# Optimization experiments

Measured on AMD Instinct MI355X. Metric: run time of the kernel, lower is better.

Reference implementation:

```python
import jax, jax.numpy as jnp
import numpy as np

# 4D convolution via lax.conv_general_dilated with 4 spatial dims.
# Layout: input (N, C, D, H, W, T), kernel (O, I, d, h, w, t).
DN = ('NCDHWT', 'OIDHWT', 'NCDHWT')


def conv4d(x, w, b, pad):
    # torch Conv2d/Conv4d is cross-correlation, matching lax.conv_general_dilated
    y = jax.lax.conv_general_dilated(
        x, w, window_strides=(1, 1, 1, 1),
        padding=[(pad, pad)] * 4, dimension_numbers=DN)
    return y + b.reshape(1, -1, 1, 1, 1, 1)


def _kaiming(key, shape):
    fan_out = shape[0] * int(np.prod(shape[2:]))
    std = np.sqrt(2.0 / fan_out)
    return (jax.random.normal(key, shape, dtype=jnp.float32) * std).astype(jnp.float32)


def setup_inputs() -> dict:
    key = jax.random.key(0)
    ks = jax.random.split(key, 11)
    B, W, H = 256, 16, 16
    corr = jax.random.normal(ks[0], (B, W * H, W, H), dtype=jnp.float32)
    w1 = _kaiming(ks[1], (1, 1, 17, 17, 9, 9))
    w2 = _kaiming(ks[2], (1, 1, 7, 7, 7, 7))
    w3 = _kaiming(ks[3], (1, 1, 5, 5, 5, 5))
    w4 = _kaiming(ks[4], (1, 1, 3, 3, 3, 3))
    w5 = _kaiming(ks[5], (1, 1, 8, 8, 1, 1))
    b1 = jax.random.normal(ks[6], (1,), dtype=jnp.float32) * 0.01
    b2 = jax.random.normal(ks[7], (1,), dtype=jnp.float32) * 0.01
    b3 = jax.random.normal(ks[8], (1,), dtype=jnp.float32) * 0.01
    b4 = jax.random.normal(ks[9], (1,), dtype=jnp.float32) * 0.01
    b5 = jax.random.normal(ks[10], (1,), dtype=jnp.float32) * 0.01
    return {"corr": corr, "w1": w1, "b1": b1, "w2": w2, "b2": b2,
            "w3": w3, "b3": b3, "w4": w4, "b4": b4, "w5": w5, "b5": b5}


def reference(corr, w1, b1, w2, b2, w3, b3, w4, b4, w5, b5):
    B, HW, W, H = corr.shape
    x = corr.reshape(B, 1, W, H, W, H)          # (B,1,16,16,16,16)
    x = jax.nn.relu(conv4d(x, w1, b1, 4))       # (B,1, 8, 8,16,16)
    x = jax.nn.relu(conv4d(x, w2, b2, 3))
    x = jax.nn.relu(conv4d(x, w3, b3, 2))
    x = jax.nn.relu(conv4d(x, w4, b4, 1))
    out = jax.nn.sigmoid(conv4d(x, w5, b5, 0))  # (B,1, 1, 1,16,16)
    return out.reshape(B, 1, W, H)
```

## Files before the change

### kernel.cpp

```cpp
#include <hip/hip_runtime.h>
#include <math.h>


typedef short bf16x8 __attribute__((ext_vector_type(8)));
typedef float f32x4 __attribute__((ext_vector_type(4)));
typedef unsigned int u32x4 __attribute__((ext_vector_type(4)));

#define XTS 64
#define NROWS 396
#define ZROW 384
#define TTS 72

__device__ __forceinline__ int xts(int row, int col) {
  return row * XTS + (col ^ ((row & 7) << 3));
}

__device__ __forceinline__ unsigned short f2bf(float f) {
  unsigned int u = __float_as_uint(f);
  u += 0x7fffu + ((u >> 16) & 1u);
  return (unsigned short)(u >> 16);
}

template <int KSZ, int PAD>
__device__ __forceinline__ void build_mid(const float* __restrict__ w,
                                          unsigned short* __restrict__ Bg, int gid) {
  const int lane = gid & 63;
  const int n_tile = (gid >> 6) & 3;
  const int chunk = (gid >> 8) & 1;
  const int tap = gid >> 9;
  const int kw = tap / KSZ, kt = tap - kw * KSZ;
  const int dh_o = n_tile * 16 + (lane & 15);
  const int d_o = dh_o >> 3, h_o = dh_o & 7;
  const int kbase = chunk * 32 + (lane >> 4) * 8;
  unsigned int pk[4];
#pragma unroll
  for (int p = 0; p < 4; ++p) {
    unsigned short half[2];
#pragma unroll
    for (int s = 0; s < 2; ++s) {
      const int k = kbase + p * 2 + s;
      const int d_i = k >> 3, h_i = k & 7;
      const int kd = d_i - d_o + PAD, kh = h_i - h_o + PAD;
      float v = 0.f;
      if (kd >= 0 && kd < KSZ && kh >= 0 && kh < KSZ)
        v = w[((kd * KSZ + kh) * KSZ + kw) * KSZ + kt];
      half[s] = f2bf(v);
    }
    pk[p] = (unsigned int)half[0] | ((unsigned int)half[1] << 16);
  }
  *(int4*)(Bg + (size_t)gid * 8) = make_int4(pk[0], pk[1], pk[2], pk[3]);
}

__global__ __launch_bounds__(256) void build_all(const float* __restrict__ w1,
                                                 const float* __restrict__ w2,
                                                 const float* __restrict__ w3,
                                                 const float* __restrict__ w4,
                                                 unsigned short* __restrict__ Bg1,
                                                 unsigned short* __restrict__ Bg2,
                                                 unsigned short* __restrict__ Bg3,
                                                 unsigned short* __restrict__ Bg4) {
  const int bid = blockIdx.x, tid = threadIdx.x;
  if (bid < 648) {
    const int gid = bid * 256 + tid;
    const int lane = gid & 63;
    const int n_tile = (gid >> 6) & 3;
    const int chunk = (gid >> 8) & 7;
    const int kwkt = gid >> 11;
    const int kw = kwkt / 9, kt = kwkt - kw * 9;
    const int dh_o = n_tile * 16 + (lane & 15);
    const int d_o = dh_o >> 3, h_o = dh_o & 7;
    const int kbase = chunk * 32 + (lane >> 4) * 8;
    unsigned int pk[4];
#pragma unroll
    for (int p = 0; p < 4; ++p) {
      unsigned short half[2];
#pragma unroll
      for (int s = 0; s < 2; ++s) {
        const int k = kbase + p * 2 + s;
        const int d_i = k >> 4, h_i = k & 15;
        const int kd = d_i - d_o + 4, kh = h_i - h_o + 4;
        float v = 0.f;
        if (kd >= 0 && kd < 17 && kh >= 0 && kh < 17)
          v = w1[((kd * 17 + kh) * 9 + kw) * 9 + kt];
        half[s] = f2bf(v);
      }
      pk[p] = (unsigned int)half[0] | ((unsigned int)half[1] << 16);
    }
    *(int4*)(Bg1 + (size_t)gid * 8) = make_int4(pk[0], pk[1], pk[2], pk[3]);
  } else if (bid < 746) {
    build_mid<7, 3>(w2, Bg2, (bid - 648) * 256 + tid);
  } else if (bid < 796) {
    build_mid<5, 2>(w3, Bg3, (bid - 746) * 256 + tid);
  } else {
    build_mid<3, 1>(w4, Bg4, (bid - 796) * 256 + tid);
  }
}

__device__ __forceinline__ void l1_load(const unsigned short* XT,
                                        const unsigned short* __restrict__ Bt,
                                        const int (&arb)[4], int kt,
                                        const int (&c0t)[8], const int (&c1t)[8],
                                        bf16x8 (&A)[8], bf16x8 (&B)[8]) {
#pragma unroll
  for (int m = 0; m < 4; ++m) {
    A[m] = *(const bf16x8*)&XT[arb[m] + kt * XTS + c0t[kt & 7]];
    A[4 + m] = *(const bf16x8*)&XT[arb[m] + kt * XTS + c1t[kt & 7]];
  }
#pragma unroll
  for (int c = 0; c < 2; ++c)
#pragma unroll
    for (int n = 0; n < 4; ++n)
      B[c * 4 + n] = *(const bf16x8*)(Bt + (size_t)kt * 16384 + c * 2048 + n * 512);
}

__device__ __forceinline__ void mfma16(const bf16x8 (&A)[8], const bf16x8 (&B)[8],
                                       f32x4 (&acc)[4][4]) {
  __builtin_amdgcn_s_setprio(1);
#pragma unroll
  for (int c = 0; c < 2; ++c)
#pragma unroll
    for (int m = 0; m < 4; ++m)
#pragma unroll
      for (int n = 0; n < 4; ++n)
        acc[m][n] = __builtin_amdgcn_mfma_f32_16x16x32_bf16(A[c * 4 + m], B[c * 4 + n],
                                                            acc[m][n], 0, 0, 0);
  __builtin_amdgcn_s_setprio(0);
}

__global__ __launch_bounds__(256) void conv_l1_mfma(const float* __restrict__ x,
                                                    const unsigned short* __restrict__ Bg,
                                                    float* __restrict__ P) {
  __shared__ __align__(16) unsigned short XT[NROWS * XTS];
  const int bx = blockIdx.x;
  const int b = bx >> 2, q = bx & 3;
  const int tid = threadIdx.x;
  const int lane = tid & 63, wave = tid >> 6;
  const int quad = lane >> 4, tl = lane & 15;
  const float* xb = x + (size_t)b * 65536;
  f32x4 acc[4][4] = {};

  int c0t[8], c1t[8];
#pragma unroll
  for (int j = 0; j < 8; ++j) {
    const int sw = ((tl + j) & 7) << 3;
    c0t[j] = (quad * 8) ^ sw;
    c1t[j] = (quad * 8 + 32) ^ sw;
  }

  for (int j = tid; j < (NROWS * XTS) / 8; j += 256)
    *(int4*)&XT[j * 8] = make_int4(0, 0, 0, 0);
  __syncthreads();

#pragma unroll
  for (int it = 0; it < 8; ++it) {
    const int i = tid + it * 256;
    const int dhp = i >> 6, wtq = i & 63;
    const int r0 = (wtq >> 2) * 24 + (wtq & 3) * 4 + 4;
    const float4 ra = *(const float4*)(xb + (size_t)(q * 64 + 2 * dhp) * 256 + wtq * 4);
    const float4 rb = *(const float4*)(xb + (size_t)(q * 64 + 2 * dhp + 1) * 256 + wtq * 4);
    const float a0[4] = {ra.x, ra.y, ra.z, ra.w};
    const float a1[4] = {rb.x, rb.y, rb.z, rb.w};
#pragma unroll
    for (int j = 0; j < 4; ++j) {
      const unsigned int p = (unsigned int)f2bf(a0[j]) | ((unsigned int)f2bf(a1[j]) << 16);
      *(unsigned int*)&XT[xts(r0 + j, dhp * 2)] = p;
    }
  }
  __syncthreads();

  const int chbase = q * 2;
  const unsigned short* Bt = Bg + (size_t)chbase * 2048 + lane * 8;
  for (int kw = 0; kw < 9; ++kw) {
    int arb[4];
#pragma unroll
    for (int m = 0; m < 4; ++m) {
      const int w_i = wave * 4 + m + kw - 4;
      arb[m] = (((unsigned)w_i < 16u) ? (w_i * 24 + tl) : ZROW) * XTS;
    }
    bf16x8 A0[8], B0[8], A1[8], B1[8];
    l1_load(XT, Bt, arb, 0, c0t, c1t, A0, B0);
#pragma unroll
    for (int kt = 0; kt < 9; ++kt) {
      if ((kt & 1) == 0) {
        if (kt < 8) l1_load(XT, Bt, arb, kt + 1, c0t, c1t, A1, B1);
        mfma16(A0, B0, acc);
      } else {
        if (kt < 8) l1_load(XT, Bt, arb, kt + 1, c0t, c1t, A0, B0);
        mfma16(A1, B1, acc);
      }
    }
    Bt += 9 * 16384;
  }

  float* Pb = P + (size_t)(q * 256 + b) * 16384;
#pragma unroll
  for (int m = 0; m < 4; ++m)
#pragma unroll
    for (int n = 0; n < 4; ++n) {
      const int dh_o = n * 16 + tl;
      const int wt0 = wave * 64 + m * 16 + quad * 4;
      *(float4*)&Pb[(size_t)dh_o * 256 + wt0] = *(const float4*)&acc[m][n];
    }
}

template <int KSZ, int PAD>
__device__ __forceinline__ void tail_load_tap(const unsigned short* XT,
                                              const unsigned short* __restrict__ Bg, int kwkt,
                                              int mw, int nh, int lane, int quad, int tl,
                                              bf16x8 (&A)[8], bf16x8 (&B)[4]) {
  const int kw = kwkt / KSZ, kt = kwkt - kw * KSZ;
  const int t_i = tl + kt - PAD;
  const bool tv = (unsigned)t_i < 16u;
  int ro[4];
#pragma unroll
  for (int m = 0; m < 4; ++m) {
    const int w_i = mw * 4 + m + kw - PAD;
    const bool v = tv && ((unsigned)w_i < 16u);
    const int row = v ? (w_i * 16 + t_i) : 256;
    ro[m] = row * TTS + quad * 8;
  }
#pragma unroll
  for (int c = 0; c < 2; ++c)
#pragma unroll
    for (int m = 0; m < 4; ++m)
      A[c * 4 + m] = *(const bf16x8*)&XT[ro[m] + c * 32];
#pragma unroll
  for (int c = 0; c < 2; ++c)
#pragma unroll
    for (int n = 0; n < 2; ++n)
      B[c * 2 + n] =
          *(const bf16x8*)(Bg + (((size_t)(kwkt * 2 + c) * 4 + (nh * 2 + n)) << 9) + lane * 8);
}

__device__ __forceinline__ void mfma8(const bf16x8 (&A)[8], const bf16x8 (&B)[4],
                                      f32x4 (&acc)[4][2]) {
  __builtin_amdgcn_s_setprio(1);
#pragma unroll
  for (int c = 0; c < 2; ++c)
#pragma unroll
    for (int m = 0; m < 4; ++m)
#pragma unroll
      for (int n = 0; n < 2; ++n)
        acc[m][n] = __builtin_amdgcn_mfma_f32_16x16x32_bf16(A[c * 4 + m], B[c * 2 + n],
                                                            acc[m][n], 0, 0, 0);
  __builtin_amdgcn_s_setprio(0);
}

template <int KSZ, int PAD, int NT>
__device__ __forceinline__ void run_layer(unsigned short* XT,
                                          const unsigned short* __restrict__ Bg,
                                          const float bias, int mw, int nh, int lane,
                                          int quad, int tl) {
  f32x4 acc[4][2] = {};
  {
    bf16x8 A0[8], B0[4], A1[8], B1[4];
    tail_load_tap<KSZ, PAD>(XT, Bg, 0, mw, nh, lane, quad, tl, A0, B0);
    int k = 0;
    while (true) {
      if (k + 1 < NT) tail_load_tap<KSZ, PAD>(XT, Bg, k + 1, mw, nh, lane, quad, tl, A1, B1);
      mfma8(A0, B0, acc);
      if (++k >= NT) break;
      if (k + 1 < NT) tail_load_tap<KSZ, PAD>(XT, Bg, k + 1, mw, nh, lane, quad, tl, A0, B0);
      mfma8(A1, B1, acc);
      if (++k >= NT) break;
    }
  }
  __syncthreads();
#pragma unroll
  for (int m = 0; m < 4; ++m)
#pragma unroll
    for (int n = 0; n < 2; ++n) {
      const int col = (nh * 2 + n) * 16 + tl;
      const int wt0 = mw * 64 + m * 16 + quad * 4;
#pragma unroll
      for (int j = 0; j < 4; ++j)
        XT[(wt0 + j) * TTS + col] = f2bf(fmaxf(acc[m][n][j] + bias, 0.f));
    }
  __syncthreads();
}

__global__ __launch_bounds__(512) void tail_fused(const float* __restrict__ P,
                                                  const unsigned short* __restrict__ Bg2,
                                                  const unsigned short* __restrict__ Bg3,
                                                  const unsigned short* __restrict__ Bg4,
                                                  const float* __restrict__ b1,
                                                  const float* __restrict__ b2,
                                                  const float* __restrict__ b3,
                                                  const float* __restrict__ b4,
                                                  const float* __restrict__ w5,
                                                  const float* __restrict__ b5,
                                                  float* __restrict__ out) {
  __shared__ __align__(16) unsigned short XT[257 * TTS];
  const int b = blockIdx.x;
  const int tid = threadIdx.x;
  const int lane = tid & 63, wave = tid >> 6;
  const int quad = lane >> 4, tl = lane & 15;
  const int mw = wave >> 1, nh = wave & 1;
  const float* p0 = P + (size_t)b * 16384;
  const float* p1 = p0 + (size_t)256 * 16384;
  const float* p2 = p0 + (size_t)512 * 16384;
  const float* p3 = p0 + (size_t)768 * 16384;
  const float bias1 = b1[0];

  if (tid < 9) *(int4*)&XT[256 * TTS + tid * 8] = make_int4(0, 0, 0, 0);
#pragma unroll
  for (int it = 0; it < 4; ++it) {
    const int i = tid + it * 512;
    const int dhp = i >> 6, wtq = i & 63;
    const size_t off0 = (size_t)(2 * dhp) * 256 + wtq * 4;
    const float4 r0a = *(const float4*)(p0 + off0);
    const float4 r0b = *(const float4*)(p1 + off0);
    const float4 r0c = *(const float4*)(p2 + off0);
    const float4 r0d = *(const float4*)(p3 + off0);
    const float4 r1a = *(const float4*)(p0 + off0 + 256);
    const float4 r1b = *(const float4*)(p1 + off0 + 256);
    const float4 r1c = *(const float4*)(p2 + off0 + 256);
    const float4 r1d = *(const float4*)(p3 + off0 + 256);
    float a0[4] = {r0a.x + r0b.x + r0c.x + r0d.x, r0a.y + r0b.y + r0c.y + r0d.y,
                   r0a.z + r0b.z + r0c.z + r0d.z, r0a.w + r0b.w + r0c.w + r0d.w};
    float a1[4] = {r1a.x + r1b.x + r1c.x + r1d.x, r1a.y + r1b.y + r1c.y + r1d.y,
                   r1a.z + r1b.z + r1c.z + r1d.z, r1a.w + r1b.w + r1c.w + r1d.w};
#pragma unroll
    for (int j = 0; j < 4; ++j) {
      const unsigned short lo = f2bf(fmaxf(a0[j] + bias1, 0.f));
      const unsigned short hi = f2bf(fmaxf(a1[j] + bias1, 0.f));
      const unsigned int p = (unsigned int)lo | ((unsigned int)hi << 16);
      *(unsigned int*)&XT[(wtq * 4 + j) * TTS + dhp * 2] = p;
    }
  }
  __syncthreads();

  run_layer<7, 3, 49>(XT, Bg2, b2[0], mw, nh, lane, quad, tl);
  run_layer<5, 2, 25>(XT, Bg3, b3[0], mw, nh, lane, quad, tl);
  run_layer<3, 1, 9>(XT, Bg4, b4[0], mw, nh, lane, quad, tl);

  if (tid < 256) {
    const int wt = tid;
    float s = b5[0];
    const unsigned short* row = &XT[wt * TTS];
#pragma unroll
    for (int k8 = 0; k8 < 8; ++k8) {
      const u32x4 v = *(const u32x4*)&row[k8 * 8];
      const unsigned int uu[4] = {(unsigned int)v.x, (unsigned int)v.y, (unsigned int)v.z,
                                  (unsigned int)v.w};
#pragma unroll
      for (int p = 0; p < 4; ++p) {
        const float lo = __uint_as_float(uu[p] << 16);
        const float hi = __uint_as_float(uu[p] & 0xFFFF0000u);
        s += lo * w5[k8 * 8 + p * 2] + hi * w5[k8 * 8 + p * 2 + 1];
      }
    }
    out[(size_t)b * 256 + wt] = 1.f / (1.f + expf(-s));
  }
}

extern "C" void kernel_launch(void* const* d_in, const int* in_sizes, int n_in,
                              void* d_out, int out_size, void* d_ws, size_t ws_size,
                              hipStream_t stream) {
  const float* corr = (const float*)d_in[0];
  const float* w1 = (const float*)d_in[1];
  const float* b1 = (const float*)d_in[2];
  const float* w2 = (const float*)d_in[3];
  const float* b2 = (const float*)d_in[4];
  const float* w3 = (const float*)d_in[5];
  const float* b3 = (const float*)d_in[6];
  const float* w4 = (const float*)d_in[7];
  const float* b4 = (const float*)d_in[8];
  const float* w5 = (const float*)d_in[9];
  const float* b5 = (const float*)d_in[10];

  float* P = (float*)d_ws;
  unsigned short* Bg1 = (unsigned short*)((char*)d_ws + (64u << 20));
  unsigned short* Bg2 = Bg1 + (size_t)81 * 8 * 4 * 64 * 8;
  unsigned short* Bg3 = Bg2 + (size_t)49 * 2 * 4 * 64 * 8;
  unsigned short* Bg4 = Bg3 + (size_t)25 * 2 * 4 * 64 * 8;

  build_all<<<814, 256, 0, stream>>>(w1, w2, w3, w4, Bg1, Bg2, Bg3, Bg4);
  conv_l1_mfma<<<1024, 256, 0, stream>>>(corr, Bg1, P);
  tail_fused<<<256, 512, 0, stream>>>(P, Bg2, Bg3, Bg4, b1, b2, b3, b4, w5, b5,
                                      (float*)d_out);
}
```

Measured before the change: 281.6 us.

## Halve layer-1 split-K partitions by looping two K-quarters per block

The layer-1 conv kernel now processes two of the four input-depth quarters per block, accumulating in registers, so only two partial-sum buffers are written instead of four. The tail kernel reads and sums two partials instead of four, cutting global write and read traffic for the partial buffers. The swizzle column offsets are now computed inline rather than held in per-thread tables, which frees registers. The cost is half as many blocks for layer 1, which reduces parallelism, plus an extra barrier between the two K passes.

Result: faster. 267.6 us (-5.0%).

```diff
diff --git a/kernel.cpp b/kernel.cpp
--- a/kernel.cpp
+++ b/kernel.cpp
@@ -98,13 +98,16 @@
 
 __device__ __forceinline__ void l1_load(const unsigned short* XT,
                                         const unsigned short* __restrict__ Bt,
-                                        const int (&arb)[4], int kt,
-                                        const int (&c0t)[8], const int (&c1t)[8],
+                                        const int (&arb)[4], int kt, int tl, int quad,
                                         bf16x8 (&A)[8], bf16x8 (&B)[8]) {
+  const int sw = ((tl + kt) & 7) << 3;
+  const int c0 = (quad * 8) ^ sw;
+  const int c1 = (quad * 8 + 32) ^ sw;
+  const int ko = kt * XTS;
 #pragma unroll
   for (int m = 0; m < 4; ++m) {
-    A[m] = *(const bf16x8*)&XT[arb[m] + kt * XTS + c0t[kt & 7]];
-    A[4 + m] = *(const bf16x8*)&XT[arb[m] + kt * XTS + c1t[kt & 7]];
+    A[m] = *(const bf16x8*)&XT[arb[m] + ko + c0];
+    A[4 + m] = *(const bf16x8*)&XT[arb[m] + ko + c1];
   }
 #pragma unroll
   for (int c = 0; c < 2; ++c)
@@ -132,67 +135,63 @@
                                                     float* __restrict__ P) {
   __shared__ __align__(16) unsigned short XT[NROWS * XTS];
   const int bx = blockIdx.x;
-  const int b = bx >> 2, q = bx & 3;
+  const int b = bx >> 1, khalf = bx & 1;
   const int tid = threadIdx.x;
   const int lane = tid & 63, wave = tid >> 6;
   const int quad = lane >> 4, tl = lane & 15;
   const float* xb = x + (size_t)b * 65536;
   f32x4 acc[4][4] = {};
 
-  int c0t[8], c1t[8];
-#pragma unroll
-  for (int j = 0; j < 8; ++j) {
-    const int sw = ((tl + j) & 7) << 3;
-    c0t[j] = (quad * 8) ^ sw;
-    c1t[j] = (quad * 8 + 32) ^ sw;
-  }
-
   for (int j = tid; j < (NROWS * XTS) / 8; j += 256)
     *(int4*)&XT[j * 8] = make_int4(0, 0, 0, 0);
   __syncthreads();
 
-#pragma unroll
-  for (int it = 0; it < 8; ++it) {
-    const int i = tid + it * 256;
-    const int dhp = i >> 6, wtq = i & 63;
-    const int r0 = (wtq >> 2) * 24 + (wtq & 3) * 4 + 4;
-    const float4 ra = *(const float4*)(xb + (size_t)(q * 64 + 2 * dhp) * 256 + wtq * 4);
-    const float4 rb = *(const float4*)(xb + (size_t)(q * 64 + 2 * dhp + 1) * 256 + wtq * 4);
-    const float a0[4] = {ra.x, ra.y, ra.z, ra.w};
-    const float a1[4] = {rb.x, rb.y, rb.z, rb.w};
-#pragma unroll
-    for (int j = 0; j < 4; ++j) {
-      const unsigned int p = (unsigned int)f2bf(a0[j]) | ((unsigned int)f2bf(a1[j]) << 16);
-      *(unsigned int*)&XT[xts(r0 + j, dhp * 2)] = p;
-    }
-  }
-  __syncthreads();
-
-  const int chbase = q * 2;
-  const unsigned short* Bt = Bg + (size_t)chbase * 2048 + lane * 8;
-  for (int kw = 0; kw < 9; ++kw) {
-    int arb[4];
-#pragma unroll
-    for (int m = 0; m < 4; ++m) {
-      const int w_i = wave * 4 + m + kw - 4;
-      arb[m] = (((unsigned)w_i < 16u) ? (w_i * 24 + tl) : ZROW) * XTS;
-    }
-    bf16x8 A0[8], B0[8], A1[8], B1[8];
-    l1_load(XT, Bt, arb, 0, c0t, c1t, A0, B0);
-#pragma unroll
-    for (int kt = 0; kt < 9; ++kt) {
-      if ((kt & 1) == 0) {
-        if (kt < 8) l1_load(XT, Bt, arb, kt + 1, c0t, c1t, A1, B1);
-        mfma16(A0, B0, acc);
-      } else {
-        if (kt < 8) l1_load(XT, Bt, arb, kt + 1, c0t, c1t, A0, B0);
-        mfma16(A1, B1, acc);
-      }
-    }
-    Bt += 9 * 16384;
-  }
-
-  float* Pb = P + (size_t)(q * 256 + b) * 16384;
+  for (int qq = 0; qq < 2; ++qq) {
+    const int q = khalf * 2 + qq;
+    if (qq) __syncthreads();
+#pragma unroll
+    for (int it = 0; it < 8; ++it) {
+      const int i = tid + it * 256;
+      const int dhp = i >> 6, wtq = i & 63;
+      const int r0 = (wtq >> 2) * 24 + (wtq & 3) * 4 + 4;
+      const float4 ra = *(const float4*)(xb + (size_t)(q * 64 + 2 * dhp) * 256 + wtq * 4);
+      const float4 rb =
+          *(const float4*)(xb + (size_t)(q * 64 + 2 * dhp + 1) * 256 + wtq * 4);
+      const float a0[4] = {ra.x, ra.y, ra.z, ra.w};
+      const float a1[4] = {rb.x, rb.y, rb.z, rb.w};
+#pragma unroll
+      for (int j = 0; j < 4; ++j) {
+        const unsigned int p = (unsigned int)f2bf(a0[j]) | ((unsigned int)f2bf(a1[j]) << 16);
+        *(unsigned int*)&XT[xts(r0 + j, dhp * 2)] = p;
+      }
+    }
+    __syncthreads();
+
+    const unsigned short* Bt = Bg + (size_t)(q * 2) * 2048 + lane * 8;
+    for (int kw = 0; kw < 9; ++kw) {
+      int arb[4];
+#pragma unroll
+      for (int m = 0; m < 4; ++m) {
+        const int w_i = wave * 4 + m + kw - 4;
+        arb[m] = (((unsigned)w_i < 16u) ? (w_i * 24 + tl) : ZROW) * XTS;
+      }
+      bf16x8 A0[8], B0[8], A1[8], B1[8];
+      l1_load(XT, Bt, arb, 0, tl, quad, A0, B0);
+#pragma unroll
+      for (int kt = 0; kt < 9; ++kt) {
+        if ((kt & 1) == 0) {
+          if (kt < 8) l1_load(XT, Bt, arb, kt + 1, tl, quad, A1, B1);
+          mfma16(A0, B0, acc);
+        } else {
+          if (kt < 8) l1_load(XT, Bt, arb, kt + 1, tl, quad, A0, B0);
+          mfma16(A1, B1, acc);
+        }
+      }
+      Bt += 9 * 16384;
+    }
+  }
+
+  float* Pb = P + (size_t)(khalf * 256 + b) * 16384;
 #pragma unroll
   for (int m = 0; m < 4; ++m)
 #pragma unroll
@@ -298,8 +297,6 @@
   const int mw = wave >> 1, nh = wave & 1;
   const float* p0 = P + (size_t)b * 16384;
   const float* p1 = p0 + (size_t)256 * 16384;
-  const float* p2 = p0 + (size_t)512 * 16384;
-  const float* p3 = p0 + (size_t)768 * 16384;
   const float bias1 = b1[0];
 
   if (tid < 9) *(int4*)&XT[256 * TTS + tid * 8] = make_int4(0, 0, 0, 0);
@@ -310,16 +307,10 @@
     const size_t off0 = (size_t)(2 * dhp) * 256 + wtq * 4;
     const float4 r0a = *(const float4*)(p0 + off0);
     const float4 r0b = *(const float4*)(p1 + off0);
-    const float4 r0c = *(const float4*)(p2 + off0);
-    const float4 r0d = *(const float4*)(p3 + off0);
     const float4 r1a = *(const float4*)(p0 + off0 + 256);
     const float4 r1b = *(const float4*)(p1 + off0 + 256);
-    const float4 r1c = *(const float4*)(p2 + off0 + 256);
-    const float4 r1d = *(const float4*)(p3 + off0 + 256);
-    float a0[4] = {r0a.x + r0b.x + r0c.x + r0d.x, r0a.y + r0b.y + r0c.y + r0d.y,
-                   r0a.z + r0b.z + r0c.z + r0d.z, r0a.w + r0b.w + r0c.w + r0d.w};
-    float a1[4] = {r1a.x + r1b.x + r1c.x + r1d.x, r1a.y + r1b.y + r1c.y + r1d.y,
-                   r1a.z + r1b.z + r1c.z + r1d.z, r1a.w + r1b.w + r1c.w + r1d.w};
+    float a0[4] = {r0a.x + r0b.x, r0a.y + r0b.y, r0a.z + r0b.z, r0a.w + r0b.w};
+    float a1[4] = {r1a.x + r1b.x, r1a.y + r1b.y, r1a.z + r1b.z, r1a.w + r1b.w};
 #pragma unroll
     for (int j = 0; j < 4; ++j) {
       const unsigned short lo = f2bf(fmaxf(a0[j] + bias1, 0.f));
@@ -376,7 +367,7 @@
   unsigned short* Bg4 = Bg3 + (size_t)25 * 2 * 4 * 64 * 8;
 
   build_all<<<814, 256, 0, stream>>>(w1, w2, w3, w4, Bg1, Bg2, Bg3, Bg4);
-  conv_l1_mfma<<<1024, 256, 0, stream>>>(corr, Bg1, P);
+  conv_l1_mfma<<<512, 256, 0, stream>>>(corr, Bg1, P);
   tail_fused<<<256, 512, 0, stream>>>(P, Bg2, Bg3, Bg4, b1, b2, b3, b4, w5, b5,
                                       (float*)d_out);
 }
```
